# Kernel optimization log

Measured on AMD Instinct MI355X. Metric: run time of the kernel, lower is better.

The kernel has to match this reference:

```python
import jax, jax.numpy as jnp
import numpy as np
import math

B = 16; L = 1024; CIN = 3; COUT = 1; D = 128; K = 16; DEPTH = 4
EPS = 1e-5; GRID_RANGE = 1.0


def _haar_basis(L):
    # Orthonormal Haar wavelet basis, rows of V (L, L). L must be power of 2.
    V = np.zeros((L, L), dtype=np.float64)
    V[0, :] = 1.0 / math.sqrt(L)
    r, s = 1, 1
    while s < L and r < L:
        block = 2 * s
        amp = 1.0 / math.sqrt(block)
        for j in range(L // block):
            st = j * block
            V[r, st:st + s] = amp
            V[r, st + s:st + block] = -amp
            r += 1
            if r >= L:
                break
        s *= 2
    return V


def _phi_f(L, k):
    # rFFT of top-k Haar basis rows, complex64 (matches build_stu_basis_rfft)
    V = _haar_basis(L)
    return jnp.asarray(np.fft.rfft(V, axis=-1)[:k].astype(np.complex64))


def setup_inputs() -> dict:
    key = jax.random.key(0)
    ks = jax.random.split(key, 8)

    def rn(k, shape, scale):
        return jax.random.normal(k, shape, dtype=jnp.float32) * scale

    return {
        "x": jax.random.normal(ks[0], (B, CIN, L), dtype=jnp.float32),
        "lift_w": rn(ks[1], (D, CIN + 1), 1.0 / math.sqrt(CIN + 1)),  # conv1x1 weight
        "lift_b": jnp.zeros((D,), jnp.float32),
        "Phi_f": _phi_f(L, K),                                        # (K, L//2+1) complex64 buffer
        "theta": rn(ks[2], (DEPTH, K, D, D), 1.0 / math.sqrt(D)),
        "ln_g": jnp.ones((DEPTH, D), jnp.float32),
        "ln_b": jnp.zeros((DEPTH, D), jnp.float32),
        "fc1_w": rn(ks[3], (DEPTH, 2 * D, D), 1.0 / math.sqrt(D)),
        "fc1_b": jnp.zeros((DEPTH, 2 * D), jnp.float32),
        "fc2_w": rn(ks[4], (DEPTH, D, 2 * D), 1.0 / math.sqrt(2 * D)),
        "fc2_b": jnp.zeros((DEPTH, D), jnp.float32),
        "head_w": rn(ks[5], (COUT, D), 1.0 / math.sqrt(D)),
        "head_b": jnp.zeros((COUT,), jnp.float32),
    }


def _forward(x, lift_w, lift_b, Phi_f, theta, ln_g, ln_b,
             fc1_w, fc1_b, fc2_w, fc2_b, head_w, head_b):
    # add_grid: append linspace coord channel -> (B, CIN+1, L)
    coords = jnp.linspace(0.0, GRID_RANGE, L, dtype=x.dtype)
    coords = jnp.broadcast_to(coords, (x.shape[0], 1, L))
    xg = jnp.concatenate([x, coords], axis=1)

    # LocalLift1D with kernel_size=1 == pointwise linear over channels
    h = jnp.einsum('bcl,dc->bdl', xg, lift_w) + lift_b[None, :, None]

    Phic = jnp.conj(Phi_f)  # (K, Lr)
    for i in range(DEPTH):
        # LayerNorm over channel dim (torch LN on transposed (B,L,D))
        mu = jnp.mean(h, axis=1, keepdims=True)
        var = jnp.var(h, axis=1, keepdims=True)
        z = (h - mu) / jnp.sqrt(var + EPS) * ln_g[i][None, :, None] + ln_b[i][None, :, None]

        Xf = jnp.fft.rfft(z, axis=-1)                       # (B, D, Lr)
        Uf = Xf[:, :, None, :] * Phic[None, None, :, :]     # (B, D, K, Lr)
        U = jnp.fft.irfft(Uf, n=L, axis=-1)                 # (B, D, K, L)

        # fused einsum('bdln,lhd->bhln') + sum over l(=k)
        S = jnp.einsum('bdkn,khd->bhn', U, theta[i])        # (B, D, L)

        # pointwise MLP (conv1x1 -> GELU -> conv1x1), residual
        H1 = jax.nn.gelu(jnp.einsum('bdl,hd->bhl', S, fc1_w[i]) + fc1_b[i][None, :, None],
                         approximate=False)
        h = h + jnp.einsum('bhl,dh->bdl', H1, fc2_w[i]) + fc2_b[i][None, :, None]

    # head: conv1x1 lifting_dim -> out_dim
    return jnp.einsum('bdl,od->bol', h, head_w) + head_b[None, :, None]


def reference(x, lift_w, lift_b, Phi_f, theta, ln_g, ln_b,
              fc1_w, fc1_b, fc2_w, fc2_b, head_w, head_b):
    return _forward(x, lift_w, lift_b, Phi_f, theta, ln_g, ln_b,
                    fc1_w, fc1_b, fc2_w, fc2_b, head_w, head_b)
```

## Files before the change

kernel.cpp:

```cpp
#include <hip/hip_runtime.h>
#include <math.h>

#define BB 16
#define LL 1024
#define DD 128
#define BL (BB*LL)
#define NDEPTH 4
#define EPSF 1e-5f

typedef unsigned short u16;
typedef short bf16x8 __attribute__((ext_vector_type(8)));
typedef short bf16x4 __attribute__((ext_vector_type(4)));
typedef float f32x4 __attribute__((ext_vector_type(4)));

static __device__ __forceinline__ u16 f2bf(float x) {
    unsigned u = __float_as_uint(x);
    u = u + 0x7fffu + ((u >> 16) & 1u);
    return (u16)(u >> 16);
}
static __device__ __forceinline__ float gelu_f(float x) {
    float u = x * 0.70710678118654752f;
    float au = fabsf(u);
    float t = __builtin_amdgcn_rcpf(1.0f + 0.3275911f * au);
    float poly = ((((1.061405429f * t - 1.453152027f) * t + 1.421413741f) * t
                   - 0.284496736f) * t + 0.254829592f) * t;
    float e = __expf(-u * u);
    float erfv = 1.0f - poly * e;
    erfv = copysignf(erfv, u);
    return 0.5f * x * (1.0f + erfv);
}

#define DZ_B  0
#define S_B   15360
#define H1_B  23552
#define RST_B 39936
#define MRS_B 40064
#define LDS_TOT 40192

#define N_TH (4*15*16384)
#define N_W1 (4*32768)
#define N_W2 (4*32768)
__global__ __launch_bounds__(256) void cvt_kernel(const float* __restrict__ theta,
        const float* __restrict__ fc1w, const float* __restrict__ fc2w,
        const float* __restrict__ ln_g,
        u16* __restrict__ thf, u16* __restrict__ w1f, u16* __restrict__ w2f) {
    int o = blockIdx.x * 256 + threadIdx.x;
    if (o < N_TH) {
        int j = o & 7, ln = (o >> 3) & 63, c = (o >> 9) & 3, f = (o >> 11) & 7;
        int slab = o >> 14;
        int layer = slab / 15, kk = slab - layer * 15;
        int h = f * 16 + (ln & 15), d = 32 * c + 8 * (ln >> 4) + j;
        float v = theta[(((size_t)layer * 16 + kk + 1) * 128 + h) * 128 + d];
        v *= ln_g[layer * 128 + d] * 0.70710678118654752f;
        thf[o] = f2bf(v);
    } else if (o < N_TH + N_W1) {
        int o2 = o - N_TH;
        int j = o2 & 7, ln = (o2 >> 3) & 63, c = (o2 >> 9) & 3, f = (o2 >> 11) & 15;
        int layer = o2 >> 15;
        int m = f * 16 + (ln & 15), d = 32 * c + 8 * (ln >> 4) + j;
        w1f[o2] = f2bf(fc1w[(size_t)layer * 32768 + m * 128 + d]);
    } else if (o < N_TH + N_W1 + N_W2) {
        int o2 = o - (N_TH + N_W1);
        int j = o2 & 7, ln = (o2 >> 3) & 63, c = (o2 >> 9) & 7, f = (o2 >> 12) & 7;
        int layer = o2 >> 15;
        int d = f * 16 + (ln & 15), m = 32 * c + 8 * (ln >> 4) + j;
        w2f[o2] = f2bf(fc2w[(size_t)layer * 32768 + d * 256 + m]);
    }
}

__global__ __launch_bounds__(512) void prep0_kernel(const float* __restrict__ x,
        const float* __restrict__ lw, const float* __restrict__ lb,
        float* __restrict__ H, float2* __restrict__ stats,
        float* __restrict__ P1p, float* __restrict__ P2p) {
    __shared__ char lds[16384 + 256];
    float* rst = (float*)(lds + 16384);
    float* mrs = (float*)(lds + 16384 + 128);
    int b = blockIdx.y, nblk = blockIdx.x, t0 = nblk * 32, tid = threadIdx.x;

    #pragma unroll
    for (int it = 0; it < 2; ++it) {
        int idx = it * 512 + tid;
        int r = idx >> 5, d0 = (idx & 31) * 4;
        int l = t0 + r;
        float x0 = x[(size_t)b * 3072 + l];
        float x1 = x[(size_t)b * 3072 + 1024 + l];
        float x2 = x[(size_t)b * 3072 + 2048 + l];
        float coord = (float)l * (1.0f / 1023.0f);
        f32x4 hv;
        #pragma unroll
        for (int q = 0; q < 4; ++q) {
            int d = d0 + q;
            float4 w = *(const float4*)(lw + d * 4);
            hv[q] = lb[d] + w.x * x0 + w.y * x1 + w.z * x2 + w.w * coord;
        }
        *(f32x4*)(H + ((size_t)b * 1024 + l) * 128 + d0) = hv;
        int byte = r * 512 + ((d0 * 4) ^ ((r & 7) << 4));
        *(f32x4*)(lds + byte) = hv;
    }
    __syncthreads();
    {
        int t = tid >> 4, q = tid & 15;
        float s = 0.f, sq = 0.f;
        #pragma unroll
        for (int dd = 0; dd < 8; dd += 4) {
            int d = q * 8 + dd;
            int byte = t * 512 + ((d * 4) ^ ((t & 7) << 4));
            f32x4 v = *(const f32x4*)(lds + byte);
            s += v[0] + v[1] + v[2] + v[3];
            sq += v[0]*v[0] + v[1]*v[1] + v[2]*v[2] + v[3]*v[3];
        }
        #pragma unroll
        for (int o = 1; o < 16; o <<= 1) {
            s += __shfl_xor(s, o, 64); sq += __shfl_xor(sq, o, 64);
        }
        if (q == 0) {
            float mu = s * (1.f / 128.f);
            float var = sq * (1.f / 128.f) - mu * mu;
            float rs = rsqrtf(var + EPSF);
            stats[(size_t)b * 1024 + t0 + t] = make_float2(mu, rs);
            rst[t] = rs; mrs[t] = mu * rs;
        }
    }
    __syncthreads();
    if (tid < 128) {
        float s = 0.f;
        #pragma unroll 8
        for (int t = 0; t < 32; ++t) {
            int byte = t * 512 + ((tid * 4) ^ ((t & 7) << 4));
            s += *(const float*)(lds + byte) * rst[t];
        }
        P1p[((size_t)b * 32 + nblk) * 128 + tid] = s;
    } else if (tid == 128) {
        float s = 0.f;
        for (int t = 0; t < 32; ++t) s += mrs[t];
        P2p[b * 32 + nblk] = s;
    }
}

__global__ __launch_bounds__(128) void c_kernel(const float* __restrict__ theta0,
        const float* __restrict__ P1p, const float* __restrict__ P2p,
        const float* __restrict__ lng, const float* __restrict__ lnb,
        float* __restrict__ C) {
    __shared__ float zsum[128];
    int b = blockIdx.x, hc = blockIdx.y, tid = threadIdx.x;
    float s = 0.f;
    #pragma unroll 8
    for (int j = 0; j < 32; ++j) s += P1p[((size_t)b * 32 + j) * 128 + tid];
    float p2 = 0.f;
    #pragma unroll 8
    for (int j = 0; j < 32; ++j) p2 += P2p[b * 32 + j];
    zsum[tid] = lng[tid] * (s - p2) + 1024.0f * lnb[tid];
    __syncthreads();
    int h = hc * 16 + (tid >> 3), q = tid & 7;
    const float* th = theta0 + h * 128 + q * 16;
    float acc = 0.f;
    #pragma unroll
    for (int d = 0; d < 16; d += 4) {
        float4 tv = *(const float4*)(th + d);
        acc += tv.x * zsum[q*16 + d] + tv.y * zsum[q*16 + d + 1]
             + tv.z * zsum[q*16 + d + 2] + tv.w * zsum[q*16 + d + 3];
    }
    acc += __shfl_xor(acc, 1, 64);
    acc += __shfl_xor(acc, 2, 64);
    acc += __shfl_xor(acc, 4, 64);
    if (q == 0) C[b * 128 + h] = acc * (1.0f / 32.0f);
}

template<int LAST>
__global__ __launch_bounds__(512, 4) void mega_kernel(
        const float* __restrict__ Hin, const float2* __restrict__ stin,
        const u16* __restrict__ thf, const float* __restrict__ Cb_,
        const u16* __restrict__ w1f, const float* __restrict__ b1,
        const u16* __restrict__ w2f, const float* __restrict__ b2,
        float* __restrict__ Hout, float2* __restrict__ stout,
        float* __restrict__ P1p, float* __restrict__ P2p,
        const float* __restrict__ hwp, const float* __restrict__ hbp,
        float* __restrict__ out) {
    __shared__ char lds[LDS_TOT];
    int b = blockIdx.y, nblk = blockIdx.x, n0 = nblk * 32, tid = threadIdx.x;

    const float* Hb = Hin + (size_t)b * 1024 * 128;
    const float2* stb = stin + (size_t)b * 1024;
    for (int c = tid; c < 60 * 16; c += 512) {
        int r = c >> 4, d0 = (c & 15) * 8;
        int gr = (n0 + r) & 1023, g1 = (n0 + r + 1) & 1023;
        const float* ha = Hb + (size_t)gr * 128 + d0;
        const float* hc = Hb + (size_t)g1 * 128 + d0;
        float2 sa = stb[gr], sb = stb[g1];
        u16 tmp[8];
        #pragma unroll
        for (int j = 0; j < 8; ++j) {
            float za = (ha[j] - sa.x) * sa.y;
            float zc = (hc[j] - sb.x) * sb.y;
            tmp[j] = f2bf(za - zc);
        }
        int byte = r * 256 + ((d0 * 2) ^ ((r & 7) << 4));
        *(bf16x8*)(lds + byte) = *(bf16x8*)tmp;
    }
    __syncthreads();

    int wave = tid >> 6, lane = tid & 63;
    int lm = lane & 15, lk = (lane >> 4) * 8;
    int fb = (wave & 3) * 2;
    int tw0 = (wave >> 2) * 16;
    f32x4 zero4 = {0.f, 0.f, 0.f, 0.f};

    f32x4 accS[2] = {zero4, zero4};
    {
        const u16* thl = thf + (size_t)lane * 8;
        #pragma unroll 4
        for (int it = 0; it < 60; ++it) {
            int kk = it >> 2, c4 = it & 3;
            bf16x8 afr0 = *(const bf16x8*)(thl + ((size_t)((kk * 8 + fb + 0) * 4 + c4) << 9));
            bf16x8 afr1 = *(const bf16x8*)(thl + ((size_t)((kk * 8 + fb + 1) * 4 + c4) << 9));
            int trow = tw0 + lm + 2 * kk;
            int byte = trow * 256 + (((c4 * 32 + lk) * 2) ^ ((trow & 7) << 4));
            bf16x8 bfr = *(const bf16x8*)(lds + byte);
            accS[0] = __builtin_amdgcn_mfma_f32_16x16x32_bf16(afr0, bfr, accS[0], 0, 0, 0);
            accS[1] = __builtin_amdgcn_mfma_f32_16x16x32_bf16(afr1, bfr, accS[1], 0, 0, 0);
        }
    }

    {
        const float* Crow = Cb_ + b * 128;
        int tl = tw0 + lm;
        #pragma unroll
        for (int mt = 0; mt < 2; ++mt) {
            int h0 = (fb + mt) * 16 + (lane >> 4) * 4;
            f32x4 cv = *(const f32x4*)(Crow + h0);
            u16 o[4];
            #pragma unroll
            for (int r = 0; r < 4; ++r) o[r] = f2bf(accS[mt][r] + cv[r]);
            int byte = S_B + tl * 256 + ((h0 * 2) ^ ((tl & 7) << 4));
            *(bf16x4*)(lds + byte) = *(bf16x4*)o;
        }
    }
    __syncthreads();

    {
        f32x4 acc1[2][2];
        #pragma unroll
        for (int mt = 0; mt < 2; ++mt)
            #pragma unroll
            for (int nt = 0; nt < 2; ++nt) acc1[mt][nt] = zero4;
        const u16* w1l = w1f + (size_t)lane * 8;
        #pragma unroll
        for (int c4 = 0; c4 < 4; ++c4) {
            bf16x8 afr[2], bfr[2];
            #pragma unroll
            for (int mt = 0; mt < 2; ++mt)
                afr[mt] = *(const bf16x8*)(w1l + ((size_t)((wave * 2 + mt) * 4 + c4) << 9));
            #pragma unroll
            for (int nt = 0; nt < 2; ++nt) {
                int tl = nt * 16 + lm;
                int byte = S_B + tl * 256 + (((c4 * 32 + lk) * 2) ^ ((tl & 7) << 4));
                bfr[nt] = *(const bf16x8*)(lds + byte);
            }
            #pragma unroll
            for (int mt = 0; mt < 2; ++mt)
                #pragma unroll
                for (int nt = 0; nt < 2; ++nt)
                    acc1[mt][nt] = __builtin_amdgcn_mfma_f32_16x16x32_bf16(
                        afr[mt], bfr[nt], acc1[mt][nt], 0, 0, 0);
        }
        #pragma unroll
        for (int mt = 0; mt < 2; ++mt) {
            int mo = wave * 32 + mt * 16 + (lane >> 4) * 4;
            f32x4 bb4 = *(const f32x4*)(b1 + mo);
            #pragma unroll
            for (int nt = 0; nt < 2; ++nt) {
                int tl = nt * 16 + lm;
                u16 o[4];
                #pragma unroll
                for (int r = 0; r < 4; ++r)
                    o[r] = f2bf(gelu_f(acc1[mt][nt][r] + bb4[r]));
                int byte = H1_B + tl * 512 + ((mo * 2) ^ ((tl & 7) << 4));
                *(bf16x4*)(lds + byte) = *(bf16x4*)o;
            }
        }
    }
    __syncthreads();

    f32x4 acc2[2] = {zero4, zero4};
    {
        const u16* w2l = w2f + (size_t)lane * 8;
        #pragma unroll
        for (int c8 = 0; c8 < 8; ++c8) {
            bf16x8 afr = *(const bf16x8*)(w2l + ((size_t)(wave * 8 + c8) << 9));
            #pragma unroll
            for (int nt = 0; nt < 2; ++nt) {
                int tl = nt * 16 + lm;
                int byte = H1_B + tl * 512 + (((c8 * 32 + lk) * 2) ^ ((tl & 7) << 4));
                bf16x8 bfr = *(const bf16x8*)(lds + byte);
                acc2[nt] = __builtin_amdgcn_mfma_f32_16x16x32_bf16(afr, bfr, acc2[nt], 0, 0, 0);
            }
        }
    }
    __syncthreads();

    {
        int dbase = wave * 16 + (lane >> 4) * 4;
        #pragma unroll
        for (int nt = 0; nt < 2; ++nt) {
            int tl = nt * 16 + lm;
            int byte = H1_B + tl * 512 + ((dbase * 4) ^ ((tl & 7) << 4));
            *(f32x4*)(lds + byte) = acc2[nt];
        }
    }
    __syncthreads();

    {
        const float* Hrow = Hin + ((size_t)b * 1024 + n0) * 128;
        float* Horow = Hout + ((size_t)b * 1024 + n0) * 128;
        #pragma unroll
        for (int it = 0; it < 2; ++it) {
            int idx = it * 512 + tid;
            int r = idx >> 5, d0 = (idx & 31) * 4;
            int byte = H1_B + r * 512 + ((d0 * 4) ^ ((r & 7) << 4));
            f32x4 v = *(const f32x4*)(lds + byte);
            f32x4 bb = *(const f32x4*)(b2 + d0);
            f32x4 hv = *(const f32x4*)(Hrow + (size_t)r * 128 + d0);
            hv = hv + v + bb;
            if (LAST) {
                f32x4 wv = *(const f32x4*)(hwp + d0);
                float s = hv[0]*wv[0] + hv[1]*wv[1] + hv[2]*wv[2] + hv[3]*wv[3];
                #pragma unroll
                for (int o = 1; o < 32; o <<= 1) s += __shfl_xor(s, o, 64);
                if ((lane & 31) == 0) out[(size_t)b * 1024 + n0 + r] = s + hbp[0];
            } else {
                *(f32x4*)(Horow + (size_t)r * 128 + d0) = hv;
                *(f32x4*)(lds + byte) = hv;
            }
        }
    }
    if (!LAST) {
        __syncthreads();
        float* rst = (float*)(lds + RST_B);
        float* mrs = (float*)(lds + MRS_B);
        {
            int t = tid >> 4, q = tid & 15;
            float s = 0.f, sq = 0.f;
            #pragma unroll
            for (int dd = 0; dd < 8; dd += 4) {
                int d = q * 8 + dd;
                int byte = H1_B + t * 512 + ((d * 4) ^ ((t & 7) << 4));
                f32x4 v = *(const f32x4*)(lds + byte);
                s += v[0] + v[1] + v[2] + v[3];
                sq += v[0]*v[0] + v[1]*v[1] + v[2]*v[2] + v[3]*v[3];
            }
            #pragma unroll
            for (int o = 1; o < 16; o <<= 1) {
                s += __shfl_xor(s, o, 64); sq += __shfl_xor(sq, o, 64);
            }
            if (q == 0) {
                float mu = s * (1.f / 128.f);
                float var = sq * (1.f / 128.f) - mu * mu;
                float rs = rsqrtf(var + EPSF);
                stout[(size_t)b * 1024 + n0 + t] = make_float2(mu, rs);
                rst[t] = rs; mrs[t] = mu * rs;
            }
        }
        __syncthreads();
        if (tid < 128) {
            float s = 0.f;
            #pragma unroll 8
            for (int t = 0; t < 32; ++t) {
                int byte = H1_B + t * 512 + ((tid * 4) ^ ((t & 7) << 4));
                s += *(const float*)(lds + byte) * rst[t];
            }
            P1p[((size_t)b * 32 + nblk) * 128 + tid] = s;
        } else if (tid == 128) {
            float s = 0.f;
            for (int t = 0; t < 32; ++t) s += mrs[t];
            P2p[b * 32 + nblk] = s;
        }
    }
}

extern "C" void kernel_launch(void* const* d_in, const int* in_sizes, int n_in,
                              void* d_out, int out_size, void* d_ws, size_t ws_size,
                              hipStream_t stream) {
    const float* x     = (const float*)d_in[0];
    const float* lw    = (const float*)d_in[1];
    const float* lb    = (const float*)d_in[2];
    const float* theta = (const float*)d_in[4];
    const float* ln_g  = (const float*)d_in[5];
    const float* ln_b  = (const float*)d_in[6];
    const float* fc1w  = (const float*)d_in[7];
    const float* fc1b  = (const float*)d_in[8];
    const float* fc2w  = (const float*)d_in[9];
    const float* fc2b  = (const float*)d_in[10];
    const float* hw    = (const float*)d_in[11];
    const float* hb    = (const float*)d_in[12];

    float* ws = (float*)d_ws;
    float* H_A = ws;
    float* H_B = H_A + (size_t)BL * DD;
    float2* st_A = (float2*)(H_B + (size_t)BL * DD);
    float2* st_B = st_A + BL;
    float* P1p = (float*)(st_B + BL);
    float* P2p = P1p + 16 * 32 * 128;
    float* Cb  = P2p + 512;
    u16* thf = (u16*)(Cb + 2048);
    u16* w1f = thf + N_TH;
    u16* w2f = w1f + N_W1;

    cvt_kernel<<<(N_TH + N_W1 + N_W2) / 256, 256, 0, stream>>>(
        theta, fc1w, fc2w, ln_g, thf, w1f, w2f);
    prep0_kernel<<<dim3(32, 16), 512, 0, stream>>>(x, lw, lb, H_A, st_A, P1p, P2p);

    float* Hi = H_A; float* Ho = H_B;
    float2* sti = st_A; float2* sto = st_B;
    for (int i = 0; i < NDEPTH; ++i) {
        c_kernel<<<dim3(16, 8), 128, 0, stream>>>(theta + (size_t)i * 16 * 16384, P1p, P2p,
                                                  ln_g + i * 128, ln_b + i * 128, Cb);
        if (i < NDEPTH - 1) {
            mega_kernel<0><<<dim3(32, 16), 512, 0, stream>>>(
                Hi, sti,
                thf + (size_t)i * 15 * 16384, Cb,
                w1f + (size_t)i * 32768, fc1b + i * 256,
                w2f + (size_t)i * 32768, fc2b + i * 128,
                Ho, sto, P1p, P2p, hw, hb, (float*)d_out);
        } else {
            mega_kernel<1><<<dim3(32, 16), 512, 0, stream>>>(
                Hi, sti,
                thf + (size_t)i * 15 * 16384, Cb,
                w1f + (size_t)i * 32768, fc1b + i * 256,
                w2f + (size_t)i * 32768, fc2b + i * 128,
                Ho, sto, P1p, P2p, hw, hb, (float*)d_out);
        }
        float* tH = Hi; Hi = Ho; Ho = tH;
        float2* tS = sti; sti = sto; sto = tS;
    }
}
```

Measured before the change: 135.2 us.

## Switch spectral GEMM to 32x32x16 MFMA with split-K across waves

Re-lays out the theta weights for 32x32x16 bf16 MFMA tiles and restructures the spectral-conv GEMM so each wave owns a 32-row h slice and half of the K reduction. Two independent accumulators hide MFMA latency, and partial sums from the second half are reduced through LDS before the bias add and bf16 store. The LDS swizzle is widened to 16 rows to match the new access pattern. This adds an extra barrier and LDS round trip for the split-K reduction, and leaves half the waves idle during the epilogue.

```diff
diff --git a/kernel.cpp b/kernel.cpp
--- a/kernel.cpp
+++ b/kernel.cpp
@@ -12,6 +12,7 @@
 typedef short bf16x8 __attribute__((ext_vector_type(8)));
 typedef short bf16x4 __attribute__((ext_vector_type(4)));
 typedef float f32x4 __attribute__((ext_vector_type(4)));
+typedef float f32x16 __attribute__((ext_vector_type(16)));
 
 static __device__ __forceinline__ u16 f2bf(float x) {
     unsigned u = __float_as_uint(x);
@@ -46,10 +47,10 @@
         u16* __restrict__ thf, u16* __restrict__ w1f, u16* __restrict__ w2f) {
     int o = blockIdx.x * 256 + threadIdx.x;
     if (o < N_TH) {
-        int j = o & 7, ln = (o >> 3) & 63, c = (o >> 9) & 3, f = (o >> 11) & 7;
+        int j = o & 7, ln = (o >> 3) & 63, hf = (o >> 9) & 3, s8 = (o >> 11) & 7;
         int slab = o >> 14;
         int layer = slab / 15, kk = slab - layer * 15;
-        int h = f * 16 + (ln & 15), d = 32 * c + 8 * (ln >> 4) + j;
+        int h = hf * 32 + (ln & 31), d = s8 * 16 + (ln >> 5) * 8 + j;
         float v = theta[(((size_t)layer * 16 + kk + 1) * 128 + h) * 128 + d];
         v *= ln_g[layer * 128 + d] * 0.70710678118654752f;
         thf[o] = f2bf(v);
@@ -194,44 +195,68 @@
             float zc = (hc[j] - sb.x) * sb.y;
             tmp[j] = f2bf(za - zc);
         }
-        int byte = r * 256 + ((d0 * 2) ^ ((r & 7) << 4));
+        int byte = r * 256 + ((d0 * 2) ^ ((r & 15) << 4));
         *(bf16x8*)(lds + byte) = *(bf16x8*)tmp;
     }
     __syncthreads();
 
     int wave = tid >> 6, lane = tid & 63;
     int lm = lane & 15, lk = (lane >> 4) * 8;
-    int fb = (wave & 3) * 2;
-    int tw0 = (wave >> 2) * 16;
     f32x4 zero4 = {0.f, 0.f, 0.f, 0.f};
 
-    f32x4 accS[2] = {zero4, zero4};
+    int hf = wave & 3, ks = wave >> 2;
+    f32x16 accA = {0.f}, accB = {0.f};
     {
         const u16* thl = thf + (size_t)lane * 8;
+        int s0 = ks * 60;
+        int l31 = lane & 31, lh = (lane >> 5) * 8;
         #pragma unroll 4
-        for (int it = 0; it < 60; ++it) {
-            int kk = it >> 2, c4 = it & 3;
-            bf16x8 afr0 = *(const bf16x8*)(thl + ((size_t)((kk * 8 + fb + 0) * 4 + c4) << 9));
-            bf16x8 afr1 = *(const bf16x8*)(thl + ((size_t)((kk * 8 + fb + 1) * 4 + c4) << 9));
-            int trow = tw0 + lm + 2 * kk;
-            int byte = trow * 256 + (((c4 * 32 + lk) * 2) ^ ((trow & 7) << 4));
-            bf16x8 bfr = *(const bf16x8*)(lds + byte);
-            accS[0] = __builtin_amdgcn_mfma_f32_16x16x32_bf16(afr0, bfr, accS[0], 0, 0, 0);
-            accS[1] = __builtin_amdgcn_mfma_f32_16x16x32_bf16(afr1, bfr, accS[1], 0, 0, 0);
-        }
-    }
-
-    {
+        for (int s = s0; s < s0 + 60; s += 2) {
+            {
+                int kk = s >> 3, s8 = s & 7;
+                bf16x8 afr = *(const bf16x8*)(thl + ((size_t)((kk * 8 + s8) * 4 + hf) << 9));
+                int trow = l31 + 2 * kk;
+                int d0 = s8 * 16 + lh;
+                int byte = trow * 256 + ((d0 * 2) ^ ((trow & 15) << 4));
+                bf16x8 bfr = *(const bf16x8*)(lds + byte);
+                accA = __builtin_amdgcn_mfma_f32_32x32x16_bf16(afr, bfr, accA, 0, 0, 0);
+            }
+            {
+                int s1 = s + 1;
+                int kk = s1 >> 3, s8 = s1 & 7;
+                bf16x8 afr = *(const bf16x8*)(thl + ((size_t)((kk * 8 + s8) * 4 + hf) << 9));
+                int trow = l31 + 2 * kk;
+                int d0 = s8 * 16 + lh;
+                int byte = trow * 256 + ((d0 * 2) ^ ((trow & 15) << 4));
+                bf16x8 bfr = *(const bf16x8*)(lds + byte);
+                accB = __builtin_amdgcn_mfma_f32_32x32x16_bf16(afr, bfr, accB, 0, 0, 0);
+            }
+        }
+    }
+    if (ks) {
+        #pragma unroll
+        for (int g = 0; g < 4; ++g) {
+            f32x4 p;
+            #pragma unroll
+            for (int r = 0; r < 4; ++r) p[r] = accA[4*g + r] + accB[4*g + r];
+            *(f32x4*)(lds + H1_B + hf * 4096 + g * 1024 + lane * 16) = p;
+        }
+    }
+    __syncthreads();
+
+    if (!ks) {
         const float* Crow = Cb_ + b * 128;
-        int tl = tw0 + lm;
-        #pragma unroll
-        for (int mt = 0; mt < 2; ++mt) {
-            int h0 = (fb + mt) * 16 + (lane >> 4) * 4;
+        int t = lane & 31;
+        #pragma unroll
+        for (int g = 0; g < 4; ++g) {
+            f32x4 p = *(const f32x4*)(lds + H1_B + hf * 4096 + g * 1024 + lane * 16);
+            int h0 = hf * 32 + g * 8 + 4 * (lane >> 5);
             f32x4 cv = *(const f32x4*)(Crow + h0);
             u16 o[4];
             #pragma unroll
-            for (int r = 0; r < 4; ++r) o[r] = f2bf(accS[mt][r] + cv[r]);
-            int byte = S_B + tl * 256 + ((h0 * 2) ^ ((tl & 7) << 4));
+            for (int r = 0; r < 4; ++r)
+                o[r] = f2bf(accA[4*g + r] + accB[4*g + r] + p[r] + cv[r]);
+            int byte = S_B + t * 256 + ((h0 * 2) ^ ((t & 7) << 4));
             *(bf16x4*)(lds + byte) = *(bf16x4*)o;
         }
     }
```

After: 140.5 us. +3.9%, slower.

## Fold per-layer C computation into producer kernels via last-block atomic counter

Applied to the files above, without the earlier changes.

Removes the separate c_kernel launch before each layer. The last block per batch, detected with an atomic counter, now computes the C bias vector for the next layer inside prep0_kernel or mega_kernel. C is double-buffered, and the counters are zeroed with a memset at launch start. This saves four small kernel launches and their serialization gaps, at the cost of a fence, an atomic per block, and a tail of serial work done by one block per batch.

```diff
diff --git a/kernel.cpp b/kernel.cpp
--- a/kernel.cpp
+++ b/kernel.cpp
@@ -36,6 +36,31 @@
 #define RST_B 39936
 #define MRS_B 40064
 #define LDS_TOT 40192
+
+static __device__ void compute_C(int b, const float* __restrict__ P1p,
+        const float* __restrict__ P2p, const float* __restrict__ lng,
+        const float* __restrict__ lnb, const float* __restrict__ th0,
+        float* __restrict__ Cout, float* zsum_lds, int tid) {
+    if (tid < 128) {
+        float s = 0.f;
+        #pragma unroll 8
+        for (int j = 0; j < 32; ++j) s += P1p[((size_t)b * 32 + j) * 128 + tid];
+        float p2 = 0.f;
+        #pragma unroll 8
+        for (int j = 0; j < 32; ++j) p2 += P2p[b * 32 + j];
+        zsum_lds[tid] = lng[tid] * (s - p2) + 1024.0f * lnb[tid];
+    }
+    __syncthreads();
+    int h = tid >> 2, q = tid & 3;
+    const float* th = th0 + h * 128 + q * 32;
+    const float* zs = zsum_lds + q * 32;
+    float acc = 0.f;
+    #pragma unroll 8
+    for (int j = 0; j < 32; ++j) acc += th[j] * zs[j];
+    acc += __shfl_xor(acc, 1, 64);
+    acc += __shfl_xor(acc, 2, 64);
+    if (q == 0) Cout[b * 128 + h] = acc * (1.0f / 32.0f);
+}
 
 #define N_TH (4*15*16384)
 #define N_W1 (4*32768)
@@ -71,8 +96,12 @@
 __global__ __launch_bounds__(512) void prep0_kernel(const float* __restrict__ x,
         const float* __restrict__ lw, const float* __restrict__ lb,
         float* __restrict__ H, float2* __restrict__ stats,
-        float* __restrict__ P1p, float* __restrict__ P2p) {
+        float* __restrict__ P1p, float* __restrict__ P2p,
+        const float* __restrict__ th0, const float* __restrict__ lng,
+        const float* __restrict__ lnb, float* __restrict__ Cout,
+        int* __restrict__ cnt) {
     __shared__ char lds[16384 + 256];
+    __shared__ int winflag;
     float* rst = (float*)(lds + 16384);
     float* mrs = (float*)(lds + 16384 + 128);
     int b = blockIdx.y, nblk = blockIdx.x, t0 = nblk * 32, tid = threadIdx.x;
@@ -135,35 +164,17 @@
         for (int t = 0; t < 32; ++t) s += mrs[t];
         P2p[b * 32 + nblk] = s;
     }
-}
-
-__global__ __launch_bounds__(128) void c_kernel(const float* __restrict__ theta0,
-        const float* __restrict__ P1p, const float* __restrict__ P2p,
-        const float* __restrict__ lng, const float* __restrict__ lnb,
-        float* __restrict__ C) {
-    __shared__ float zsum[128];
-    int b = blockIdx.x, hc = blockIdx.y, tid = threadIdx.x;
-    float s = 0.f;
-    #pragma unroll 8
-    for (int j = 0; j < 32; ++j) s += P1p[((size_t)b * 32 + j) * 128 + tid];
-    float p2 = 0.f;
-    #pragma unroll 8
-    for (int j = 0; j < 32; ++j) p2 += P2p[b * 32 + j];
-    zsum[tid] = lng[tid] * (s - p2) + 1024.0f * lnb[tid];
-    __syncthreads();
-    int h = hc * 16 + (tid >> 3), q = tid & 7;
-    const float* th = theta0 + h * 128 + q * 16;
-    float acc = 0.f;
-    #pragma unroll
-    for (int d = 0; d < 16; d += 4) {
-        float4 tv = *(const float4*)(th + d);
-        acc += tv.x * zsum[q*16 + d] + tv.y * zsum[q*16 + d + 1]
-             + tv.z * zsum[q*16 + d + 2] + tv.w * zsum[q*16 + d + 3];
-    }
-    acc += __shfl_xor(acc, 1, 64);
-    acc += __shfl_xor(acc, 2, 64);
-    acc += __shfl_xor(acc, 4, 64);
-    if (q == 0) C[b * 128 + h] = acc * (1.0f / 32.0f);
+    __syncthreads();
+    __threadfence();
+    if (tid == 0) {
+        int old = __hip_atomic_fetch_add(&cnt[b], 1, __ATOMIC_ACQ_REL, __HIP_MEMORY_SCOPE_AGENT);
+        winflag = (old == 31);
+    }
+    __syncthreads();
+    if (winflag) {
+        __threadfence();
+        compute_C(b, P1p, P2p, lng, lnb, th0, Cout, (float*)lds, tid);
+    }
 }
 
 template<int LAST>
@@ -175,8 +186,12 @@
         float* __restrict__ Hout, float2* __restrict__ stout,
         float* __restrict__ P1p, float* __restrict__ P2p,
         const float* __restrict__ hwp, const float* __restrict__ hbp,
-        float* __restrict__ out) {
+        float* __restrict__ out,
+        const float* __restrict__ th0n, const float* __restrict__ lngn,
+        const float* __restrict__ lnbn, float* __restrict__ Cnext,
+        int* __restrict__ cnt) {
     __shared__ char lds[LDS_TOT];
+    __shared__ int winflag;
     int b = blockIdx.y, nblk = blockIdx.x, n0 = nblk * 32, tid = threadIdx.x;
 
     const float* Hb = Hin + (size_t)b * 1024 * 128;
@@ -374,6 +389,17 @@
             for (int t = 0; t < 32; ++t) s += mrs[t];
             P2p[b * 32 + nblk] = s;
         }
+        __syncthreads();
+        __threadfence();
+        if (tid == 0) {
+            int old = __hip_atomic_fetch_add(&cnt[b], 1, __ATOMIC_ACQ_REL, __HIP_MEMORY_SCOPE_AGENT);
+            winflag = (old == 31);
+        }
+        __syncthreads();
+        if (winflag) {
+            __threadfence();
+            compute_C(b, P1p, P2p, lngn, lnbn, th0n, Cnext, (float*)lds, tid);
+        }
     }
 }
 
@@ -400,36 +426,45 @@
     float2* st_B = st_A + BL;
     float* P1p = (float*)(st_B + BL);
     float* P2p = P1p + 16 * 32 * 128;
-    float* Cb  = P2p + 512;
-    u16* thf = (u16*)(Cb + 2048);
+    float* Cb0 = P2p + 512;
+    float* Cb1 = Cb0 + 2048;
+    int*   cnt = (int*)(Cb1 + 2048);
+    u16* thf = (u16*)(cnt + 64);
     u16* w1f = thf + N_TH;
     u16* w2f = w1f + N_W1;
 
+    hipMemsetAsync(cnt, 0, 64 * sizeof(int), stream);
     cvt_kernel<<<(N_TH + N_W1 + N_W2) / 256, 256, 0, stream>>>(
         theta, fc1w, fc2w, ln_g, thf, w1f, w2f);
-    prep0_kernel<<<dim3(32, 16), 512, 0, stream>>>(x, lw, lb, H_A, st_A, P1p, P2p);
+    prep0_kernel<<<dim3(32, 16), 512, 0, stream>>>(
+        x, lw, lb, H_A, st_A, P1p, P2p,
+        theta , ln_g, ln_b, Cb0, cnt + 0);
 
     float* Hi = H_A; float* Ho = H_B;
     float2* sti = st_A; float2* sto = st_B;
+    float* Ci = Cb0; float* Co = Cb1;
     for (int i = 0; i < NDEPTH; ++i) {
-        c_kernel<<<dim3(16, 8), 128, 0, stream>>>(theta + (size_t)i * 16 * 16384, P1p, P2p,
-                                                  ln_g + i * 128, ln_b + i * 128, Cb);
         if (i < NDEPTH - 1) {
             mega_kernel<0><<<dim3(32, 16), 512, 0, stream>>>(
                 Hi, sti,
-                thf + (size_t)i * 15 * 16384, Cb,
+                thf + (size_t)i * 15 * 16384, Ci,
                 w1f + (size_t)i * 32768, fc1b + i * 256,
                 w2f + (size_t)i * 32768, fc2b + i * 128,
-                Ho, sto, P1p, P2p, hw, hb, (float*)d_out);
+                Ho, sto, P1p, P2p, hw, hb, (float*)d_out,
+                theta + (size_t)(i + 1) * 16 * 16384,
+                ln_g + (i + 1) * 128, ln_b + (i + 1) * 128,
+                Co, cnt + 16 * (1 + i));
         } else {
             mega_kernel<1><<<dim3(32, 16), 512, 0, stream>>>(
                 Hi, sti,
-                thf + (size_t)i * 15 * 16384, Cb,
+                thf + (size_t)i * 15 * 16384, Ci,
                 w1f + (size_t)i * 32768, fc1b + i * 256,
                 w2f + (size_t)i * 32768, fc2b + i * 128,
-                Ho, sto, P1p, P2p, hw, hb, (float*)d_out);
+                Ho, sto, P1p, P2p, hw, hb, (float*)d_out,
+                theta, ln_g, ln_b, Co, cnt);
         }
         float* tH = Hi; Hi = Ho; Ho = tH;
         float2* tS = sti; sti = sto; sto = tS;
-    }
-}
+        float* tC = Ci; Ci = Co; Co = tC;
+    }
+}
```

After: 483.9 us. 258% more time.

## Halve per-block sequence tile to 16 rows with 256-thread blocks

Applied to the files above, without the earlier changes.

Each block in prep0 and the per-layer mega kernel now covers 16 sequence positions with 4 waves instead of 32 positions with 8 waves, so the grid doubles to 64x16 blocks. The MFMA work split per wave is reorganised: each wave owns more output rows for a single 16-column tile in the fc1/fc2 stages. LDS shrinks, and the partial-sum buffers grow to 64 slices, which the c_kernel reduction now walks. The aim is more blocks for the 256 CUs and better occupancy. The costs are a larger relative halo (44 rows loaded for 16 outputs versus 60 for 32), more weight-fragment loads per unit of work, and a longer reduction.

```diff
diff --git a/kernel.cpp b/kernel.cpp
--- a/kernel.cpp
+++ b/kernel.cpp
@@ -31,11 +31,11 @@
 }
 
 #define DZ_B  0
-#define S_B   15360
-#define H1_B  23552
-#define RST_B 39936
-#define MRS_B 40064
-#define LDS_TOT 40192
+#define S_B   11264
+#define H1_B  15360
+#define RST_B 23552
+#define MRS_B 23616
+#define LDS_TOT 23680
 
 #define N_TH (4*15*16384)
 #define N_W1 (4*32768)
@@ -68,18 +68,18 @@
     }
 }
 
-__global__ __launch_bounds__(512) void prep0_kernel(const float* __restrict__ x,
+__global__ __launch_bounds__(256) void prep0_kernel(const float* __restrict__ x,
         const float* __restrict__ lw, const float* __restrict__ lb,
         float* __restrict__ H, float2* __restrict__ stats,
         float* __restrict__ P1p, float* __restrict__ P2p) {
-    __shared__ char lds[16384 + 256];
-    float* rst = (float*)(lds + 16384);
-    float* mrs = (float*)(lds + 16384 + 128);
-    int b = blockIdx.y, nblk = blockIdx.x, t0 = nblk * 32, tid = threadIdx.x;
+    __shared__ char lds[8192 + 128];
+    float* rst = (float*)(lds + 8192);
+    float* mrs = (float*)(lds + 8192 + 64);
+    int b = blockIdx.y, nblk = blockIdx.x, t0 = nblk * 16, tid = threadIdx.x;
 
     #pragma unroll
     for (int it = 0; it < 2; ++it) {
-        int idx = it * 512 + tid;
+        int idx = it * 256 + tid;
         int r = idx >> 5, d0 = (idx & 31) * 4;
         int l = t0 + r;
         float x0 = x[(size_t)b * 3072 + l];
@@ -124,16 +124,16 @@
     __syncthreads();
     if (tid < 128) {
         float s = 0.f;
-        #pragma unroll 8
-        for (int t = 0; t < 32; ++t) {
+        #pragma unroll
+        for (int t = 0; t < 16; ++t) {
             int byte = t * 512 + ((tid * 4) ^ ((t & 7) << 4));
             s += *(const float*)(lds + byte) * rst[t];
         }
-        P1p[((size_t)b * 32 + nblk) * 128 + tid] = s;
+        P1p[((size_t)b * 64 + nblk) * 128 + tid] = s;
     } else if (tid == 128) {
         float s = 0.f;
-        for (int t = 0; t < 32; ++t) s += mrs[t];
-        P2p[b * 32 + nblk] = s;
+        for (int t = 0; t < 16; ++t) s += mrs[t];
+        P2p[b * 64 + nblk] = s;
     }
 }
 
@@ -145,10 +145,10 @@
     int b = blockIdx.x, hc = blockIdx.y, tid = threadIdx.x;
     float s = 0.f;
     #pragma unroll 8
-    for (int j = 0; j < 32; ++j) s += P1p[((size_t)b * 32 + j) * 128 + tid];
+    for (int j = 0; j < 64; ++j) s += P1p[((size_t)b * 64 + j) * 128 + tid];
     float p2 = 0.f;
     #pragma unroll 8
-    for (int j = 0; j < 32; ++j) p2 += P2p[b * 32 + j];
+    for (int j = 0; j < 64; ++j) p2 += P2p[b * 64 + j];
     zsum[tid] = lng[tid] * (s - p2) + 1024.0f * lnb[tid];
     __syncthreads();
     int h = hc * 16 + (tid >> 3), q = tid & 7;
@@ -167,7 +167,7 @@
 }
 
 template<int LAST>
-__global__ __launch_bounds__(512, 4) void mega_kernel(
+__global__ __launch_bounds__(256, 4) void mega_kernel(
         const float* __restrict__ Hin, const float2* __restrict__ stin,
         const u16* __restrict__ thf, const float* __restrict__ Cb_,
         const u16* __restrict__ w1f, const float* __restrict__ b1,
@@ -177,11 +177,11 @@
         const float* __restrict__ hwp, const float* __restrict__ hbp,
         float* __restrict__ out) {
     __shared__ char lds[LDS_TOT];
-    int b = blockIdx.y, nblk = blockIdx.x, n0 = nblk * 32, tid = threadIdx.x;
+    int b = blockIdx.y, nblk = blockIdx.x, n0 = nblk * 16, tid = threadIdx.x;
 
     const float* Hb = Hin + (size_t)b * 1024 * 128;
     const float2* stb = stin + (size_t)b * 1024;
-    for (int c = tid; c < 60 * 16; c += 512) {
+    for (int c = tid; c < 44 * 16; c += 256) {
         int r = c >> 4, d0 = (c & 15) * 8;
         int gr = (n0 + r) & 1023, g1 = (n0 + r + 1) & 1023;
         const float* ha = Hb + (size_t)gr * 128 + d0;
@@ -201,8 +201,7 @@
 
     int wave = tid >> 6, lane = tid & 63;
     int lm = lane & 15, lk = (lane >> 4) * 8;
-    int fb = (wave & 3) * 2;
-    int tw0 = (wave >> 2) * 16;
+    int fb = wave * 2;
     f32x4 zero4 = {0.f, 0.f, 0.f, 0.f};
 
     f32x4 accS[2] = {zero4, zero4};
@@ -213,7 +212,7 @@
             int kk = it >> 2, c4 = it & 3;
             bf16x8 afr0 = *(const bf16x8*)(thl + ((size_t)((kk * 8 + fb + 0) * 4 + c4) << 9));
             bf16x8 afr1 = *(const bf16x8*)(thl + ((size_t)((kk * 8 + fb + 1) * 4 + c4) << 9));
-            int trow = tw0 + lm + 2 * kk;
+            int trow = lm + 2 * kk;
             int byte = trow * 256 + (((c4 * 32 + lk) * 2) ^ ((trow & 7) << 4));
             bf16x8 bfr = *(const bf16x8*)(lds + byte);
             accS[0] = __builtin_amdgcn_mfma_f32_16x16x32_bf16(afr0, bfr, accS[0], 0, 0, 0);
@@ -223,7 +222,7 @@
 
     {
         const float* Crow = Cb_ + b * 128;
-        int tl = tw0 + lm;
+        int tl = lm;
         #pragma unroll
         for (int mt = 0; mt < 2; ++mt) {
             int h0 = (fb + mt) * 16 + (lane >> 4) * 4;
@@ -238,73 +237,60 @@
     __syncthreads();
 
     {
-        f32x4 acc1[2][2];
-        #pragma unroll
-        for (int mt = 0; mt < 2; ++mt)
-            #pragma unroll
-            for (int nt = 0; nt < 2; ++nt) acc1[mt][nt] = zero4;
+        f32x4 acc1[4];
+        #pragma unroll
+        for (int mt = 0; mt < 4; ++mt) acc1[mt] = zero4;
         const u16* w1l = w1f + (size_t)lane * 8;
         #pragma unroll
         for (int c4 = 0; c4 < 4; ++c4) {
-            bf16x8 afr[2], bfr[2];
+            bf16x8 afr[4];
+            #pragma unroll
+            for (int mt = 0; mt < 4; ++mt)
+                afr[mt] = *(const bf16x8*)(w1l + ((size_t)((wave * 4 + mt) * 4 + c4) << 9));
+            int byte = S_B + lm * 256 + (((c4 * 32 + lk) * 2) ^ ((lm & 7) << 4));
+            bf16x8 bfr = *(const bf16x8*)(lds + byte);
+            #pragma unroll
+            for (int mt = 0; mt < 4; ++mt)
+                acc1[mt] = __builtin_amdgcn_mfma_f32_16x16x32_bf16(afr[mt], bfr, acc1[mt], 0, 0, 0);
+        }
+        #pragma unroll
+        for (int mt = 0; mt < 4; ++mt) {
+            int mo = wave * 64 + mt * 16 + (lane >> 4) * 4;
+            f32x4 bb4 = *(const f32x4*)(b1 + mo);
+            u16 o[4];
+            #pragma unroll
+            for (int r = 0; r < 4; ++r)
+                o[r] = f2bf(gelu_f(acc1[mt][r] + bb4[r]));
+            int byte = H1_B + lm * 512 + ((mo * 2) ^ ((lm & 7) << 4));
+            *(bf16x4*)(lds + byte) = *(bf16x4*)o;
+        }
+    }
+    __syncthreads();
+
+    f32x4 acc2[2] = {zero4, zero4};
+    {
+        const u16* w2l = w2f + (size_t)lane * 8;
+        #pragma unroll
+        for (int c8 = 0; c8 < 8; ++c8) {
+            bf16x8 afr[2];
             #pragma unroll
             for (int mt = 0; mt < 2; ++mt)
-                afr[mt] = *(const bf16x8*)(w1l + ((size_t)((wave * 2 + mt) * 4 + c4) << 9));
-            #pragma unroll
-            for (int nt = 0; nt < 2; ++nt) {
-                int tl = nt * 16 + lm;
-                int byte = S_B + tl * 256 + (((c4 * 32 + lk) * 2) ^ ((tl & 7) << 4));
-                bfr[nt] = *(const bf16x8*)(lds + byte);
-            }
+                afr[mt] = *(const bf16x8*)(w2l + ((size_t)((wave * 2 + mt) * 8 + c8) << 9));
+            int byte = H1_B + lm * 512 + (((c8 * 32 + lk) * 2) ^ ((lm & 7) << 4));
+            bf16x8 bfr = *(const bf16x8*)(lds + byte);
             #pragma unroll
             for (int mt = 0; mt < 2; ++mt)
-                #pragma unroll
-                for (int nt = 0; nt < 2; ++nt)
-                    acc1[mt][nt] = __builtin_amdgcn_mfma_f32_16x16x32_bf16(
-                        afr[mt], bfr[nt], acc1[mt][nt], 0, 0, 0);
-        }
+                acc2[mt] = __builtin_amdgcn_mfma_f32_16x16x32_bf16(afr[mt], bfr, acc2[mt], 0, 0, 0);
+        }
+    }
+    __syncthreads();
+
+    {
         #pragma unroll
         for (int mt = 0; mt < 2; ++mt) {
-            int mo = wave * 32 + mt * 16 + (lane >> 4) * 4;
-            f32x4 bb4 = *(const f32x4*)(b1 + mo);
-            #pragma unroll
-            for (int nt = 0; nt < 2; ++nt) {
-                int tl = nt * 16 + lm;
-                u16 o[4];
-                #pragma unroll
-                for (int r = 0; r < 4; ++r)
-                    o[r] = f2bf(gelu_f(acc1[mt][nt][r] + bb4[r]));
-                int byte = H1_B + tl * 512 + ((mo * 2) ^ ((tl & 7) << 4));
-                *(bf16x4*)(lds + byte) = *(bf16x4*)o;
-            }
-        }
-    }
-    __syncthreads();
-
-    f32x4 acc2[2] = {zero4, zero4};
-    {
-        const u16* w2l = w2f + (size_t)lane * 8;
-        #pragma unroll
-        for (int c8 = 0; c8 < 8; ++c8) {
-            bf16x8 afr = *(const bf16x8*)(w2l + ((size_t)(wave * 8 + c8) << 9));
-            #pragma unroll
-            for (int nt = 0; nt < 2; ++nt) {
-                int tl = nt * 16 + lm;
-                int byte = H1_B + tl * 512 + (((c8 * 32 + lk) * 2) ^ ((tl & 7) << 4));
-                bf16x8 bfr = *(const bf16x8*)(lds + byte);
-                acc2[nt] = __builtin_amdgcn_mfma_f32_16x16x32_bf16(afr, bfr, acc2[nt], 0, 0, 0);
-            }
-        }
-    }
-    __syncthreads();
-
-    {
-        int dbase = wave * 16 + (lane >> 4) * 4;
-        #pragma unroll
-        for (int nt = 0; nt < 2; ++nt) {
-            int tl = nt * 16 + lm;
-            int byte = H1_B + tl * 512 + ((dbase * 4) ^ ((tl & 7) << 4));
-            *(f32x4*)(lds + byte) = acc2[nt];
+            int dbase = wave * 32 + mt * 16 + (lane >> 4) * 4;
+            int byte = H1_B + lm * 512 + ((dbase * 4) ^ ((lm & 7) << 4));
+            *(f32x4*)(lds + byte) = acc2[mt];
         }
     }
     __syncthreads();
@@ -314,7 +300,7 @@
         float* Horow = Hout + ((size_t)b * 1024 + n0) * 128;
         #pragma unroll
         for (int it = 0; it < 2; ++it) {
-            int idx = it * 512 + tid;
+            int idx = it * 256 + tid;
             int r = idx >> 5, d0 = (idx & 31) * 4;
             int byte = H1_B + r * 512 + ((d0 * 4) ^ ((r & 7) << 4));
             f32x4 v = *(const f32x4*)(lds + byte);
@@ -363,16 +349,16 @@
         __syncthreads();
         if (tid < 128) {
             float s = 0.f;
-            #pragma unroll 8
-            for (int t = 0; t < 32; ++t) {
+            #pragma unroll
+            for (int t = 0; t < 16; ++t) {
                 int byte = H1_B + t * 512 + ((tid * 4) ^ ((t & 7) << 4));
                 s += *(const float*)(lds + byte) * rst[t];
             }
-            P1p[((size_t)b * 32 + nblk) * 128 + tid] = s;
+            P1p[((size_t)b * 64 + nblk) * 128 + tid] = s;
         } else if (tid == 128) {
             float s = 0.f;
-            for (int t = 0; t < 32; ++t) s += mrs[t];
-            P2p[b * 32 + nblk] = s;
+            for (int t = 0; t < 16; ++t) s += mrs[t];
+            P2p[b * 64 + nblk] = s;
         }
     }
 }
@@ -399,15 +385,15 @@
     float2* st_A = (float2*)(H_B + (size_t)BL * DD);
     float2* st_B = st_A + BL;
     float* P1p = (float*)(st_B + BL);
-    float* P2p = P1p + 16 * 32 * 128;
-    float* Cb  = P2p + 512;
+    float* P2p = P1p + 16 * 64 * 128;
+    float* Cb  = P2p + 1024;
     u16* thf = (u16*)(Cb + 2048);
     u16* w1f = thf + N_TH;
     u16* w2f = w1f + N_W1;
 
     cvt_kernel<<<(N_TH + N_W1 + N_W2) / 256, 256, 0, stream>>>(
         theta, fc1w, fc2w, ln_g, thf, w1f, w2f);
-    prep0_kernel<<<dim3(32, 16), 512, 0, stream>>>(x, lw, lb, H_A, st_A, P1p, P2p);
+    prep0_kernel<<<dim3(64, 16), 256, 0, stream>>>(x, lw, lb, H_A, st_A, P1p, P2p);
 
     float* Hi = H_A; float* Ho = H_B;
     float2* sti = st_A; float2* sto = st_B;
@@ -415,14 +401,14 @@
         c_kernel<<<dim3(16, 8), 128, 0, stream>>>(theta + (size_t)i * 16 * 16384, P1p, P2p,
                                                   ln_g + i * 128, ln_b + i * 128, Cb);
         if (i < NDEPTH - 1) {
-            mega_kernel<0><<<dim3(32, 16), 512, 0, stream>>>(
+            mega_kernel<0><<<dim3(64, 16), 256, 0, stream>>>(
                 Hi, sti,
                 thf + (size_t)i * 15 * 16384, Cb,
                 w1f + (size_t)i * 32768, fc1b + i * 256,
                 w2f + (size_t)i * 32768, fc2b + i * 128,
                 Ho, sto, P1p, P2p, hw, hb, (float*)d_out);
         } else {
-            mega_kernel<1><<<dim3(32, 16), 512, 0, stream>>>(
+            mega_kernel<1><<<dim3(64, 16), 256, 0, stream>>>(
                 Hi, sti,
                 thf + (size_t)i * 15 * 16384, Cb,
                 w1f + (size_t)i * 32768, fc1b + i * 256,
```

After: 150.8 us. 1.12x slower.
